# Optimization experiments

Measured on AMD Instinct MI355X. Metric: run time of the kernel, lower is better.

Reference implementation:

```python
import jax, jax.numpy as jnp
import numpy as np

DECAY = 0.99
EPS = 1e-10
COMMIT = 0.25
K = 1024
D = 64


def setup_inputs() -> dict:
    key = jax.random.key(0)
    k1, k2, k3, k4 = jax.random.split(key, 4)
    return {
        "z_e": jax.random.normal(k1, (64, 64, 32, 32), dtype=jnp.float32),
        "embedding_w": jax.random.normal(k2, (K, D), dtype=jnp.float32),
        "ema_cluster_size": jax.random.uniform(k3, (K,), dtype=jnp.float32),
        "ema_w": jax.random.normal(k4, (K, D), dtype=jnp.float32),
    }


def reference(z_e, embedding_w, ema_cluster_size, ema_w):
    # [B, C, H, W] -> [B, H, W, C] -> [N, D]
    z_nhwc = jnp.transpose(z_e, (0, 2, 3, 1))
    z_flat = z_nhwc.reshape(-1, z_nhwc.shape[-1])

    # Squared-euclidean distances via ||z||^2 + ||e||^2 - 2 z e^T  -> [N, K]
    z_sq = jnp.sum(z_flat * z_flat, axis=1, keepdims=True)
    e_sq = jnp.sum(embedding_w * embedding_w, axis=1)
    distances = z_sq + e_sq - 2.0 * (z_flat @ embedding_w.T)

    indices = jnp.argmin(distances, axis=1)                      # [N]
    encodings = jax.nn.one_hot(indices, K, dtype=z_flat.dtype)   # [N, K]

    quantized = embedding_w[indices].reshape(z_nhwc.shape)       # [B, H, W, C]

    # --- EMA codebook update (training path; no-grad in original) ---
    counts = jnp.sum(encodings, axis=0)                          # [K]
    new_cluster_size = DECAY * ema_cluster_size + (1.0 - DECAY) * counts
    dw = encodings.T @ z_flat                                    # [K, D]
    new_ema_w = DECAY * ema_w + (1.0 - DECAY) * dw
    n = jnp.sum(new_cluster_size)
    cluster_size = (new_cluster_size + EPS) / (n + K * EPS) * n
    new_embedding_w = new_ema_w / cluster_size[:, None]

    # Commitment loss (quantized detached)
    diff = jax.lax.stop_gradient(quantized) - z_nhwc
    loss = COMMIT * jnp.mean(diff * diff)

    # Straight-through estimator
    quantized_st = z_nhwc + jax.lax.stop_gradient(quantized - z_nhwc)

    avg_probs = jnp.mean(encodings, axis=0)
    perplexity = jnp.exp(-jnp.sum(avg_probs * jnp.log(avg_probs + 1e-10)))

    quantized_out = jnp.transpose(quantized_st, (0, 3, 1, 2))    # [B, C, H, W]
    return (quantized_out, loss, perplexity, encodings,
            new_embedding_w, new_cluster_size, new_ema_w)
```

## Files before the change

### kernel.cpp

```cpp
#include <hip/hip_runtime.h>
#include <math.h>

#define NTOT 65536
#define KCB  1024
#define DIM  64

typedef float fvec2 __attribute__((ext_vector_type(2)));
typedef float fvec4 __attribute__((ext_vector_type(4)));
typedef short sh8  __attribute__((ext_vector_type(8)));

static const size_t OFF_Q    = 0;
static const size_t OFF_LOSS = 4194304;
static const size_t OFF_PERP = 4194305;
static const size_t OFF_ENC  = 4194306;
static const size_t OFF_EMB  = 71303170;
static const size_t OFF_NCS  = 71368706;
static const size_t OFF_NEMA = 71369730;

static const size_t WSO_IDX   = 0;
static const size_t WSO_ESQ   = 262144;
static const size_t WSO_LOSSP = 266240;
static const size_t WSO_CNT   = 270336;
static const size_t WSO_SCAL  = 274432;
static const size_t WSO_EBH   = 278528;
static const size_t WSO_EBL   = 409600;
static const size_t WSO_PDW   = 540672;
static const size_t WSO_PCNT  = 4734976;
static const size_t WSO_ZC    = 4800512;
static const size_t WS_NEED_ZC = 4800512 + (size_t)NTOT * DIM * 4;

__device__ __forceinline__ unsigned short f2bf(float f) {
    unsigned u = __builtin_bit_cast(unsigned, f);
    return (unsigned short)((u + 0x7FFFu + ((u >> 16) & 1u)) >> 16);
}
__device__ __forceinline__ float bf2f(unsigned short h) {
    unsigned u = ((unsigned)h) << 16;
    return __builtin_bit_cast(float, u);
}

__global__ void k_eprep(const float* __restrict__ emb,
                        unsigned short* __restrict__ ebh,
                        unsigned short* __restrict__ ebl,
                        float* __restrict__ esq) {
    int gid = blockIdx.x * 256 + threadIdx.x;
    int c = gid >> 3, ko8 = gid & 7;
    const fvec4* p = (const fvec4*)(emb + ((size_t)c << 6) + (ko8 << 3));
    fvec4 v0 = p[0], v1 = p[1];
    float f[8] = {v0.x, v0.y, v0.z, v0.w, v1.x, v1.y, v1.z, v1.w};
    sh8 h, l;
    float sq0 = 0.f, sq1 = 0.f;
#pragma unroll
    for (int j = 0; j < 8; ++j) {
        unsigned short hb = f2bf(f[j]);
        h[j] = (short)hb;
        l[j] = (short)f2bf(f[j] - bf2f(hb));
        if (j < 4) sq0 = fmaf(f[j], f[j], sq0); else sq1 = fmaf(f[j], f[j], sq1);
    }
    float sq = sq0 + sq1;
    sq += __shfl_xor(sq, 1, 64);
    sq += __shfl_xor(sq, 2, 64);
    sq += __shfl_xor(sq, 4, 64);
    if (ko8 == 0) esq[c] = sq;

    int ct = c >> 4, cl = c & 15, kc = ko8 >> 2, ko = ko8 & 3;
    size_t base = ((((size_t)ct << 1) + kc) << 9) + (((size_t)(ko << 4) + cl) << 3);
    *(sh8*)(ebh + base) = h;
    *(sh8*)(ebl + base) = l;
}

__global__ __launch_bounds__(256, 4)
void k_assign(const float* __restrict__ ze, const float* __restrict__ emb,
              const float* __restrict__ esq,
              const unsigned short* __restrict__ ebh,
              const unsigned short* __restrict__ ebl,
              int* __restrict__ idx_out, float* __restrict__ lossp,
              float* __restrict__ zc, int use_zc) {
    __shared__ float zt[4096];
    __shared__ float etq[4096];
    __shared__ int   sfidx[64];

    const int tid  = threadIdx.x;
    const int blk  = blockIdx.x;
    const int b    = blk >> 4;
    const int hw0  = (blk & 15) << 6;
    const int n0   = blk << 6;
    const int lane = tid & 63;
    const int wave = tid >> 6;
    const int cg   = lane & 15;
    const int ko   = lane >> 4;

#pragma unroll
    for (int j = 0; j < 4; ++j) {
        int idx = tid + (j << 8);
        int d = idx >> 4, r0 = (idx & 15) << 2;
        const fvec4 v = *(const fvec4*)(ze + (((size_t)(b << 6) + d) << 10) + hw0 + r0);
        zt[(r0 + 0) * 64 + d] = v.x;
        zt[(r0 + 1) * 64 + d] = v.y;
        zt[(r0 + 2) * 64 + d] = v.z;
        zt[(r0 + 3) * 64 + d] = v.w;
    }
    __syncthreads();

    const int arow = (wave << 4) + cg;
    sh8 Ah0, Ah1, Al0, Al1;
#pragma unroll
    for (int j = 0; j < 8; ++j) {
        float f0 = zt[arow * 64 + (ko << 3) + j];
        float f1 = zt[arow * 64 + 32 + (ko << 3) + j];
        unsigned short h0 = f2bf(f0), h1 = f2bf(f1);
        Ah0[j] = (short)h0;  Al0[j] = (short)f2bf(f0 - bf2f(h0));
        Ah1[j] = (short)h1;  Al1[j] = (short)f2bf(f1 - bf2f(h1));
    }

    float tb[4]  = {3.4e38f, 3.4e38f, 3.4e38f, 3.4e38f};
    float ts2[4] = {3.4e38f, 3.4e38f, 3.4e38f, 3.4e38f};
    int ti1[4] = {0, 0, 0, 0};
    int ti2[4] = {0, 0, 0, 0};

    const size_t lb = (size_t)lane << 3;
#define LOADB(d0, d1, d2, d3, ctv)                                  \
    { size_t o_ = ((size_t)(ctv) << 10) + lb;                       \
      d0 = *(const sh8*)(ebh + o_);                                 \
      d1 = *(const sh8*)(ebh + o_ + 512);                           \
      d2 = *(const sh8*)(ebl + o_);                                 \
      d3 = *(const sh8*)(ebl + o_ + 512); }

#define FOLD(ctv, acc)                                              \
    { const int code_ = ((ctv) << 4) + cg;                          \
      const float es_ = esq[code_];                                 \
      _Pragma("unroll")                                             \
      for (int rg = 0; rg < 4; ++rg) {                              \
          float s_ = fmaf((acc)[rg], -2.0f, es_);                   \
          bool c1 = s_ < tb[rg];                                    \
          bool c2 = s_ < ts2[rg];                                   \
          ti2[rg] = c1 ? ti1[rg] : (c2 ? code_ : ti2[rg]);          \
          ts2[rg] = c1 ? tb[rg] : (c2 ? s_ : ts2[rg]);              \
          ti1[rg] = c1 ? code_ : ti1[rg];                           \
          tb[rg]  = c1 ? s_ : tb[rg];                               \
      } }

#define TILE(i) ((((i) + (blk << 1)) & 63))

    sh8 b0h0, b0h1, b0l0, b0l1, b1h0, b1h1, b1l0, b1l1;
    LOADB(b0h0, b0h1, b0l0, b0l1, TILE(0));
    LOADB(b1h0, b1h1, b1l0, b1l1, TILE(1));

    for (int i = 0; i < 64; i += 2) {
        fvec4 aa = {0.f, 0.f, 0.f, 0.f}, ab = {0.f, 0.f, 0.f, 0.f};
        aa = __builtin_amdgcn_mfma_f32_16x16x32_bf16(Ah0, b0h0, aa, 0, 0, 0);
        ab = __builtin_amdgcn_mfma_f32_16x16x32_bf16(Ah1, b0h1, ab, 0, 0, 0);
        aa = __builtin_amdgcn_mfma_f32_16x16x32_bf16(Ah0, b0l0, aa, 0, 0, 0);
        ab = __builtin_amdgcn_mfma_f32_16x16x32_bf16(Ah1, b0l1, ab, 0, 0, 0);
        aa = __builtin_amdgcn_mfma_f32_16x16x32_bf16(Al0, b0h0, aa, 0, 0, 0);
        ab = __builtin_amdgcn_mfma_f32_16x16x32_bf16(Al1, b0h1, ab, 0, 0, 0);
        const int ct0 = TILE(i);
        if (i + 2 < 64) LOADB(b0h0, b0h1, b0l0, b0l1, TILE(i + 2));
        fvec4 acc0 = aa + ab;
        FOLD(ct0, acc0);

        fvec4 ba = {0.f, 0.f, 0.f, 0.f}, bb = {0.f, 0.f, 0.f, 0.f};
        ba = __builtin_amdgcn_mfma_f32_16x16x32_bf16(Ah0, b1h0, ba, 0, 0, 0);
        bb = __builtin_amdgcn_mfma_f32_16x16x32_bf16(Ah1, b1h1, bb, 0, 0, 0);
        ba = __builtin_amdgcn_mfma_f32_16x16x32_bf16(Ah0, b1l0, ba, 0, 0, 0);
        bb = __builtin_amdgcn_mfma_f32_16x16x32_bf16(Ah1, b1l1, bb, 0, 0, 0);
        ba = __builtin_amdgcn_mfma_f32_16x16x32_bf16(Al0, b1h0, ba, 0, 0, 0);
        bb = __builtin_amdgcn_mfma_f32_16x16x32_bf16(Al1, b1h1, bb, 0, 0, 0);
        const int ct1 = TILE(i + 1);
        if (i + 3 < 64) LOADB(b1h0, b1h1, b1l0, b1l1, TILE(i + 3));
        fvec4 acc1 = ba + bb;
        FOLD(ct1, acc1);
    }
#undef TILE
#undef LOADB
#undef FOLD

    float* mb  = etq;
    float* ms2 = etq + 1024;
    int*   mi1 = (int*)(etq + 2048);
    int*   mi2 = (int*)(etq + 3072);
#pragma unroll
    for (int rg = 0; rg < 4; ++rg) {
        int row = (wave << 4) + (ko << 2) + rg;
        mb [(cg << 6) + row] = tb[rg];
        ms2[(cg << 6) + row] = ts2[rg];
        mi1[(cg << 6) + row] = ti1[rg];
        mi2[(cg << 6) + row] = ti2[rg];
    }
    __syncthreads();

    if (tid < 64) {
        const int r = tid;
        float fb = mb[r], fs2 = ms2[r];
        int fi1 = mi1[r], fi2 = mi2[r];
#pragma unroll
        for (int p = 1; p < 16; ++p) {
            float ob = mb[(p << 6) + r], os2 = ms2[(p << 6) + r];
            int oi1 = mi1[(p << 6) + r], oi2 = mi2[(p << 6) + r];
            if (ob < fb)       { fs2 = fb; fi2 = fi1; fb = ob; fi1 = oi1; }
            else if (ob < fs2) { fs2 = ob; fi2 = oi1; }
            if (os2 < fs2)     { fs2 = os2; fi2 = oi2; }
        }
        if (fs2 - fb < 2e-2f) {
            double d1 = 0.0, d2 = 0.0;
            const float* e1 = emb + (size_t)fi1 * 64;
            const float* e2 = emb + (size_t)fi2 * 64;
            for (int d = 0; d < 64; ++d) {
                double zd = (double)zt[r * 64 + d];
                double q1 = zd - (double)e1[d];
                double q2 = zd - (double)e2[d];
                d1 += q1 * q1;
                d2 += q2 * q2;
            }
            if ((d2 < d1) || (d2 == d1 && fi2 < fi1)) fi1 = fi2;
        }
        sfidx[r] = fi1;
        idx_out[n0 + r] = fi1;
    }
    __syncthreads();

    float lacc = 0.f;
    for (int i = tid; i < 1024; i += 256) {
        int r = i >> 4, d4 = (i & 15) << 2;
        const fvec4 zv = *(const fvec4*)&zt[(r << 6) + d4];
        const fvec4 ev = *(const fvec4*)(emb + ((size_t)sfidx[r] << 6) + d4);
        fvec4 df = ev - zv;
        lacc = fmaf(df.x, df.x, lacc);
        lacc = fmaf(df.y, df.y, lacc);
        lacc = fmaf(df.z, df.z, lacc);
        lacc = fmaf(df.w, df.w, lacc);
        if (use_zc)
            *(fvec4*)&zc[(((size_t)(n0 + r)) << 6) + d4] = zv;
    }
    __syncthreads();

    float* lred = etq;
    lred[tid] = lacc;
    __syncthreads();
    for (int s = 128; s > 0; s >>= 1) {
        if (tid < s) lred[tid] += lred[tid + s];
        __syncthreads();
    }
    if (tid == 0) lossp[blk] = lred[0];
}

__global__ __launch_bounds__(256)
void k_tail(const int* __restrict__ idx, const float* __restrict__ zcmp,
            const float* __restrict__ ze, const float* __restrict__ emb,
            float* __restrict__ out, float* __restrict__ pdw,
            int* __restrict__ pcnt, int use_zc) {
    __shared__ __align__(16) char smem[32864];
    const int t = threadIdx.x;

    if (blockIdx.x & 1) {
        const int blk = blockIdx.x >> 1;
        const int b   = blk >> 4;
        const int hw0 = (blk & 15) << 6;
        const int n0  = blk << 6;
        int*   sfidx = (int*)smem;
        float* qt    = (float*)(smem + 256);

        if (t < 64) sfidx[t] = idx[n0 + t];
        __syncthreads();

        for (int i = t; i < 4096; i += 256) {
            int r = i >> 6, d = i & 63;
            qt[d * 65 + r] = emb[(size_t)sfidx[r] * 64 + d];
        }

        float* ebase = out + OFF_ENC;
        if (t < 255) {
            const int cb = 2 + (t << 2);
            for (int r = 0; r < 64; ++r) {
                const int fi = sfidx[r];
                fvec4 v;
                v.x = (fi == cb)     ? 1.0f : 0.0f;
                v.y = (fi == cb + 1) ? 1.0f : 0.0f;
                v.z = (fi == cb + 2) ? 1.0f : 0.0f;
                v.w = (fi == cb + 3) ? 1.0f : 0.0f;
                __builtin_nontemporal_store(
                    v, (fvec4*)(ebase + ((size_t)(n0 + r) << 10) + cb));
            }
        } else {
            for (int r = 0; r < 64; ++r) {
                const int fi = sfidx[r];
                float* rowp = ebase + ((size_t)(n0 + r) << 10);
                fvec2 hd, tl;
                hd.x = (fi == 0)    ? 1.0f : 0.0f;
                hd.y = (fi == 1)    ? 1.0f : 0.0f;
                tl.x = (fi == 1022) ? 1.0f : 0.0f;
                tl.y = (fi == 1023) ? 1.0f : 0.0f;
                __builtin_nontemporal_store(hd, (fvec2*)rowp);
                __builtin_nontemporal_store(tl, (fvec2*)(rowp + 1022));
            }
        }
        __syncthreads();

        for (int i = t; i < 4096; i += 256) {
            int d = i >> 6, r = i & 63;
            __builtin_nontemporal_store(
                qt[d * 65 + r],
                &out[OFF_Q + ((size_t)((b << 6) + d) << 10) + hw0 + r]);
        }
        return;
    }

    const int sidx = blockIdx.x >> 1;
    const int kg   = sidx & 63;
    const int ng   = sidx >> 6;
    const int k0   = kg << 4;
    const int g    = t >> 6;
    const int d    = t & 63;
    const int lane = t & 63;

    int*   s_list = (int*)smem;
    float* part   = (float*)(smem + 16384);
    int*   s_wsum = (int*)(smem + 32768);
    int*   s_cnt  = (int*)(smem + 32784);

    for (int i = t; i < 4096; i += 256) part[i] = 0.f;
    if (t < 16) s_cnt[t] = 0;

    const int nb = (ng << 12) + (t << 4);
    const int4* ip = (const int4*)(idx + nb);
    const int4 v0 = ip[0], v1 = ip[1], v2 = ip[2], v3 = ip[3];

#define MM(x) ((unsigned)((x) - k0) < 16u)
    int c = 0;
    c += MM(v0.x) + MM(v0.y) + MM(v0.z) + MM(v0.w);
    c += MM(v1.x) + MM(v1.y) + MM(v1.z) + MM(v1.w);
    c += MM(v2.x) + MM(v2.y) + MM(v2.z) + MM(v2.w);
    c += MM(v3.x) + MM(v3.y) + MM(v3.z) + MM(v3.w);

    int inc = c;
#pragma unroll
    for (int off = 1; off < 64; off <<= 1) {
        int y = __shfl_up(inc, (unsigned)off, 64);
        if (lane >= off) inc += y;
    }
    if (lane == 63) s_wsum[g] = inc;
    __syncthreads();

    int wbase = 0;
#pragma unroll
    for (int w = 0; w < 4; ++w) wbase += (w < g) ? s_wsum[w] : 0;
    const int M = s_wsum[0] + s_wsum[1] + s_wsum[2] + s_wsum[3];
    int pos = wbase + inc - c;

#define EMIT(x, o) if (MM(x)) { s_list[pos++] = (((t << 4) + (o)) << 4) | ((x) - k0); \
                                atomicAdd(&s_cnt[(x) - k0], 1); }
    EMIT(v0.x, 0)  EMIT(v0.y, 1)  EMIT(v0.z, 2)  EMIT(v0.w, 3)
    EMIT(v1.x, 4)  EMIT(v1.y, 5)  EMIT(v1.z, 6)  EMIT(v1.w, 7)
    EMIT(v2.x, 8)  EMIT(v2.y, 9)  EMIT(v2.z, 10) EMIT(v2.w, 11)
    EMIT(v3.x, 12) EMIT(v3.y, 13) EMIT(v3.z, 14) EMIT(v3.w, 15)
#undef EMIT
#undef MM
    __syncthreads();

#define ZL(nloc) (use_zc ? zcmp[(((size_t)((ng << 12) + (nloc))) << 6) + d] \
                         : ze[((((size_t)(((ng << 12) + (nloc)) >> 10) << 6) + d) << 10) + (((ng << 12) + (nloc)) & 1023)])
    {
        float* pg = part + (g << 10);
        int j = g;
        for (; j + 4 < M; j += 8) {
            int e0 = s_list[j], e1 = s_list[j + 4];
            float f0 = ZL(e0 >> 4);
            float f1 = ZL(e1 >> 4);
            pg[((e0 & 15) << 6) + d] += f0;
            pg[((e1 & 15) << 6) + d] += f1;
        }
        for (; j < M; j += 4) {
            int e0 = s_list[j];
            pg[((e0 & 15) << 6) + d] += ZL(e0 >> 4);
        }
    }
#undef ZL
    __syncthreads();

    for (int i = t; i < 1024; i += 256) {
        float s = ((part[i] + part[1024 + i]) + part[2048 + i]) + part[3072 + i];
        int cc = i >> 6, dd = i & 63;
        pdw[(((size_t)(ng << 10) + k0 + cc) << 6) + dd] = s;
    }
    if (t < 16) pcnt[(ng << 10) + k0 + t] = s_cnt[t];
}

__global__ __launch_bounds__(256)
void k_red(const float* __restrict__ pdw, const int* __restrict__ pcnt,
           const float* __restrict__ emaw, const float* __restrict__ ecs,
           float* __restrict__ out, int* __restrict__ counts) {
    const int gid = blockIdx.x * 256 + threadIdx.x;
    const int k = gid >> 6, d = gid & 63;
    float s = 0.f;
#pragma unroll
    for (int ng = 0; ng < 16; ++ng)
        s += pdw[(((size_t)(ng << 10) + k) << 6) + d];
    out[OFF_NEMA + ((size_t)k << 6) + d] =
        fmaf(0.01f, s, 0.99f * emaw[((size_t)k << 6) + d]);
    if (d == 0) {
        int c = 0;
#pragma unroll
        for (int ng = 0; ng < 16; ++ng) c += pcnt[(ng << 10) + k];
        counts[k] = c;
        out[OFF_NCS + k] = fmaf(0.01f, (float)c, 0.99f * ecs[k]);
    }
}

__global__ void k_scalars(const float* __restrict__ lossp, const int* __restrict__ counts,
                          const float* __restrict__ ncs, float* __restrict__ out,
                          float* __restrict__ scal) {
    __shared__ float sr[256];
    const int t = threadIdx.x;

    float v = lossp[t] + lossp[t + 256] + lossp[t + 512] + lossp[t + 768];
    sr[t] = v;
    __syncthreads();
    for (int s = 128; s > 0; s >>= 1) { if (t < s) sr[t] += sr[t + s]; __syncthreads(); }
    if (t == 0) out[OFF_LOSS] = sr[0] * (0.25f / 4194304.0f);
    __syncthreads();

    v = ncs[t] + ncs[t + 256] + ncs[t + 512] + ncs[t + 768];
    sr[t] = v;
    __syncthreads();
    for (int s = 128; s > 0; s >>= 1) { if (t < s) sr[t] += sr[t + s]; __syncthreads(); }
    if (t == 0) scal[0] = sr[0];
    __syncthreads();

    float pv = 0.f;
    for (int i = t; i < 1024; i += 256) {
        float p = (float)counts[i] * (1.0f / 65536.0f);
        pv += p * logf(p + 1e-10f);
    }
    sr[t] = pv;
    __syncthreads();
    for (int s = 128; s > 0; s >>= 1) { if (t < s) sr[t] += sr[t + s]; __syncthreads(); }
    if (t == 0) out[OFF_PERP] = expf(-sr[0]);
}

__global__ void k_embnorm(const float* __restrict__ nema, const float* __restrict__ ncs,
                          const float* __restrict__ scal, float* __restrict__ embw) {
    int i = blockIdx.x * 256 + threadIdx.x;
    float n = scal[0];
    int k = i >> 6;
    float cs = (ncs[k] + 1e-10f) / (n + 1.024e-7f) * n;
    embw[i] = nema[i] / cs;
}

extern "C" void kernel_launch(void* const* d_in, const int* in_sizes, int n_in,
                              void* d_out, int out_size, void* d_ws, size_t ws_size,
                              hipStream_t stream) {
    const float* ze   = (const float*)d_in[0];
    const float* emb  = (const float*)d_in[1];
    const float* ecs  = (const float*)d_in[2];
    const float* emaw = (const float*)d_in[3];
    float* out = (float*)d_out;
    char*  ws  = (char*)d_ws;

    int*            idx    = (int*)(ws + WSO_IDX);
    float*          esq    = (float*)(ws + WSO_ESQ);
    float*          lossp  = (float*)(ws + WSO_LOSSP);
    int*            counts = (int*)(ws + WSO_CNT);
    float*          scal   = (float*)(ws + WSO_SCAL);
    unsigned short* ebh    = (unsigned short*)(ws + WSO_EBH);
    unsigned short* ebl    = (unsigned short*)(ws + WSO_EBL);
    float*          pdw    = (float*)(ws + WSO_PDW);
    int*            pcnt   = (int*)(ws + WSO_PCNT);
    float*          zc     = (float*)(ws + WSO_ZC);
    const int use_zc = (ws_size >= WS_NEED_ZC) ? 1 : 0;

    k_eprep  <<<32,   256, 0, stream>>>(emb, ebh, ebl, esq);
    k_assign <<<1024, 256, 0, stream>>>(ze, emb, esq, ebh, ebl, idx, lossp, zc, use_zc);
    k_tail   <<<2048, 256, 0, stream>>>(idx, zc, ze, emb, out, pdw, pcnt, use_zc);
    k_red    <<<256,  256, 0, stream>>>(pdw, pcnt, emaw, ecs, out, counts);
    k_scalars<<<1,    256, 0, stream>>>(lossp, counts, out + OFF_NCS, out, scal);
    k_embnorm<<<256,  256, 0, stream>>>(out + OFF_NEMA, out + OFF_NCS, scal, out + OFF_EMB);
}
```

Baseline: 155.1 us.

## Split assignment kernel into single-wave blocks of 16 rows with shuffle reductions

The codebook-assignment kernel moves from 256-thread blocks covering 64 rows to 64-thread single-wave blocks covering 16 rows, launched 4096 times. Cross-lane top-2 merging and the loss reduction now use wave shuffles instead of shared-memory tree reductions, which removes most barriers and shrinks LDS use so more blocks fit per CU. The explicit double-buffered codebook prefetch is dropped in favour of simple per-iteration loads. In exchange, each codebook tile is reloaded by four times as many blocks, the z loads become scalar strided reads, and the loss partial buffer grows to 4096 entries.

Measured after the change: 170.6 us. +10.0%, slower.

```diff
diff --git a/kernel.cpp b/kernel.cpp
--- a/kernel.cpp
+++ b/kernel.cpp
@@ -20,14 +20,14 @@
 static const size_t WSO_IDX   = 0;
 static const size_t WSO_ESQ   = 262144;
 static const size_t WSO_LOSSP = 266240;
-static const size_t WSO_CNT   = 270336;
-static const size_t WSO_SCAL  = 274432;
-static const size_t WSO_EBH   = 278528;
-static const size_t WSO_EBL   = 409600;
-static const size_t WSO_PDW   = 540672;
-static const size_t WSO_PCNT  = 4734976;
-static const size_t WSO_ZC    = 4800512;
-static const size_t WS_NEED_ZC = 4800512 + (size_t)NTOT * DIM * 4;
+static const size_t WSO_CNT   = 282624;
+static const size_t WSO_SCAL  = 286720;
+static const size_t WSO_EBH   = 290816;
+static const size_t WSO_EBL   = 421888;
+static const size_t WSO_PDW   = 552960;
+static const size_t WSO_PCNT  = 4747264;
+static const size_t WSO_ZC    = 4812800;
+static const size_t WS_NEED_ZC = 4812800 + (size_t)NTOT * DIM * 4;
 
 __device__ __forceinline__ unsigned short f2bf(float f) {
     unsigned u = __builtin_bit_cast(unsigned, f);
@@ -68,45 +68,40 @@
     *(sh8*)(ebl + base) = l;
 }
 
-__global__ __launch_bounds__(256, 4)
+__global__ __launch_bounds__(64, 8)
 void k_assign(const float* __restrict__ ze, const float* __restrict__ emb,
               const float* __restrict__ esq,
               const unsigned short* __restrict__ ebh,
               const unsigned short* __restrict__ ebl,
               int* __restrict__ idx_out, float* __restrict__ lossp,
               float* __restrict__ zc, int use_zc) {
-    __shared__ float zt[4096];
-    __shared__ float etq[4096];
-    __shared__ int   sfidx[64];
-
-    const int tid  = threadIdx.x;
+    __shared__ float zt[16 * 65];
+    __shared__ float sm_b[16], sm_s2[16];
+    __shared__ int   sm_i1[16], sm_i2[16], sfidx[16];
+
+    const int lane = threadIdx.x;
     const int blk  = blockIdx.x;
-    const int b    = blk >> 4;
-    const int hw0  = (blk & 15) << 6;
-    const int n0   = blk << 6;
-    const int lane = tid & 63;
-    const int wave = tid >> 6;
+    const int b    = blk >> 6;
+    const int hw0  = (blk & 63) << 4;
+    const int n0   = blk << 4;
     const int cg   = lane & 15;
     const int ko   = lane >> 4;
 
-#pragma unroll
-    for (int j = 0; j < 4; ++j) {
-        int idx = tid + (j << 8);
-        int d = idx >> 4, r0 = (idx & 15) << 2;
-        const fvec4 v = *(const fvec4*)(ze + (((size_t)(b << 6) + d) << 10) + hw0 + r0);
-        zt[(r0 + 0) * 64 + d] = v.x;
-        zt[(r0 + 1) * 64 + d] = v.y;
-        zt[(r0 + 2) * 64 + d] = v.z;
-        zt[(r0 + 3) * 64 + d] = v.w;
-    }
-    __syncthreads();
-
-    const int arow = (wave << 4) + cg;
+    {
+        const int r = lane & 15;
+        const int dq = lane >> 4;
+        for (int it = 0; it < 16; ++it) {
+            const int d = (it << 2) + dq;
+            zt[r * 65 + d] = ze[(((size_t)(b << 6) + d) << 10) + hw0 + r];
+        }
+    }
+    __syncthreads();
+
     sh8 Ah0, Ah1, Al0, Al1;
 #pragma unroll
     for (int j = 0; j < 8; ++j) {
-        float f0 = zt[arow * 64 + (ko << 3) + j];
-        float f1 = zt[arow * 64 + 32 + (ko << 3) + j];
+        float f0 = zt[cg * 65 + (ko << 3) + j];
+        float f1 = zt[cg * 65 + 32 + (ko << 3) + j];
         unsigned short h0 = f2bf(f0), h1 = f2bf(f1);
         Ah0[j] = (short)h0;  Al0[j] = (short)f2bf(f0 - bf2f(h0));
         Ah1[j] = (short)h1;  Al1[j] = (short)f2bf(f1 - bf2f(h1));
@@ -117,95 +112,75 @@
     int ti1[4] = {0, 0, 0, 0};
     int ti2[4] = {0, 0, 0, 0};
 
-    const size_t lb = (size_t)lane << 3;
-#define LOADB(d0, d1, d2, d3, ctv)                                  \
-    { size_t o_ = ((size_t)(ctv) << 10) + lb;                       \
-      d0 = *(const sh8*)(ebh + o_);                                 \
-      d1 = *(const sh8*)(ebh + o_ + 512);                           \
-      d2 = *(const sh8*)(ebl + o_);                                 \
-      d3 = *(const sh8*)(ebl + o_ + 512); }
-
-#define FOLD(ctv, acc)                                              \
-    { const int code_ = ((ctv) << 4) + cg;                          \
-      const float es_ = esq[code_];                                 \
-      _Pragma("unroll")                                             \
-      for (int rg = 0; rg < 4; ++rg) {                              \
-          float s_ = fmaf((acc)[rg], -2.0f, es_);                   \
-          bool c1 = s_ < tb[rg];                                    \
-          bool c2 = s_ < ts2[rg];                                   \
-          ti2[rg] = c1 ? ti1[rg] : (c2 ? code_ : ti2[rg]);          \
-          ts2[rg] = c1 ? tb[rg] : (c2 ? s_ : ts2[rg]);              \
-          ti1[rg] = c1 ? code_ : ti1[rg];                           \
-          tb[rg]  = c1 ? s_ : tb[rg];                               \
-      } }
-
-#define TILE(i) ((((i) + (blk << 1)) & 63))
-
-    sh8 b0h0, b0h1, b0l0, b0l1, b1h0, b1h1, b1l0, b1l1;
-    LOADB(b0h0, b0h1, b0l0, b0l1, TILE(0));
-    LOADB(b1h0, b1h1, b1l0, b1l1, TILE(1));
-
-    for (int i = 0; i < 64; i += 2) {
+    const int lb = lane << 3;
+
+    for (int i = 0; i < 64; ++i) {
+        const int ct = (i + blk) & 63;
+        const unsigned short* ph = ebh + ((size_t)ct << 10);
+        const unsigned short* pl = ebl + ((size_t)ct << 10);
+        sh8 bh0 = *(const sh8*)(ph + lb);
+        sh8 bh1 = *(const sh8*)(ph + 512 + lb);
+        sh8 bl0 = *(const sh8*)(pl + lb);
+        sh8 bl1 = *(const sh8*)(pl + 512 + lb);
+        const float es = esq[(ct << 4) + cg];
+
         fvec4 aa = {0.f, 0.f, 0.f, 0.f}, ab = {0.f, 0.f, 0.f, 0.f};
-        aa = __builtin_amdgcn_mfma_f32_16x16x32_bf16(Ah0, b0h0, aa, 0, 0, 0);
-        ab = __builtin_amdgcn_mfma_f32_16x16x32_bf16(Ah1, b0h1, ab, 0, 0, 0);
-        aa = __builtin_amdgcn_mfma_f32_16x16x32_bf16(Ah0, b0l0, aa, 0, 0, 0);
-        ab = __builtin_amdgcn_mfma_f32_16x16x32_bf16(Ah1, b0l1, ab, 0, 0, 0);
-        aa = __builtin_amdgcn_mfma_f32_16x16x32_bf16(Al0, b0h0, aa, 0, 0, 0);
-        ab = __builtin_amdgcn_mfma_f32_16x16x32_bf16(Al1, b0h1, ab, 0, 0, 0);
-        const int ct0 = TILE(i);
-        if (i + 2 < 64) LOADB(b0h0, b0h1, b0l0, b0l1, TILE(i + 2));
-        fvec4 acc0 = aa + ab;
-        FOLD(ct0, acc0);
-
-        fvec4 ba = {0.f, 0.f, 0.f, 0.f}, bb = {0.f, 0.f, 0.f, 0.f};
-        ba = __builtin_amdgcn_mfma_f32_16x16x32_bf16(Ah0, b1h0, ba, 0, 0, 0);
-        bb = __builtin_amdgcn_mfma_f32_16x16x32_bf16(Ah1, b1h1, bb, 0, 0, 0);
-        ba = __builtin_amdgcn_mfma_f32_16x16x32_bf16(Ah0, b1l0, ba, 0, 0, 0);
-        bb = __builtin_amdgcn_mfma_f32_16x16x32_bf16(Ah1, b1l1, bb, 0, 0, 0);
-        ba = __builtin_amdgcn_mfma_f32_16x16x32_bf16(Al0, b1h0, ba, 0, 0, 0);
-        bb = __builtin_amdgcn_mfma_f32_16x16x32_bf16(Al1, b1h1, bb, 0, 0, 0);
-        const int ct1 = TILE(i + 1);
-        if (i + 3 < 64) LOADB(b1h0, b1h1, b1l0, b1l1, TILE(i + 3));
-        fvec4 acc1 = ba + bb;
-        FOLD(ct1, acc1);
-    }
-#undef TILE
-#undef LOADB
-#undef FOLD
-
-    float* mb  = etq;
-    float* ms2 = etq + 1024;
-    int*   mi1 = (int*)(etq + 2048);
-    int*   mi2 = (int*)(etq + 3072);
-#pragma unroll
-    for (int rg = 0; rg < 4; ++rg) {
-        int row = (wave << 4) + (ko << 2) + rg;
-        mb [(cg << 6) + row] = tb[rg];
-        ms2[(cg << 6) + row] = ts2[rg];
-        mi1[(cg << 6) + row] = ti1[rg];
-        mi2[(cg << 6) + row] = ti2[rg];
-    }
-    __syncthreads();
-
-    if (tid < 64) {
-        const int r = tid;
-        float fb = mb[r], fs2 = ms2[r];
-        int fi1 = mi1[r], fi2 = mi2[r];
-#pragma unroll
-        for (int p = 1; p < 16; ++p) {
-            float ob = mb[(p << 6) + r], os2 = ms2[(p << 6) + r];
-            int oi1 = mi1[(p << 6) + r], oi2 = mi2[(p << 6) + r];
-            if (ob < fb)       { fs2 = fb; fi2 = fi1; fb = ob; fi1 = oi1; }
-            else if (ob < fs2) { fs2 = ob; fi2 = oi1; }
-            if (os2 < fs2)     { fs2 = os2; fi2 = oi2; }
-        }
-        if (fs2 - fb < 2e-2f) {
+        aa = __builtin_amdgcn_mfma_f32_16x16x32_bf16(Ah0, bh0, aa, 0, 0, 0);
+        ab = __builtin_amdgcn_mfma_f32_16x16x32_bf16(Ah1, bh1, ab, 0, 0, 0);
+        aa = __builtin_amdgcn_mfma_f32_16x16x32_bf16(Ah0, bl0, aa, 0, 0, 0);
+        ab = __builtin_amdgcn_mfma_f32_16x16x32_bf16(Ah1, bl1, ab, 0, 0, 0);
+        aa = __builtin_amdgcn_mfma_f32_16x16x32_bf16(Al0, bh0, aa, 0, 0, 0);
+        ab = __builtin_amdgcn_mfma_f32_16x16x32_bf16(Al1, bh1, ab, 0, 0, 0);
+        fvec4 acc = aa + ab;
+
+        const int code = (ct << 4) + cg;
+#pragma unroll
+        for (int s = 0; s < 4; ++s) {
+            float sc = fmaf(acc[s], -2.0f, es);
+            bool c1 = sc < tb[s];
+            bool c2 = sc < ts2[s];
+            ti2[s] = c1 ? ti1[s] : (c2 ? code : ti2[s]);
+            ts2[s] = c1 ? tb[s] : (c2 ? sc : ts2[s]);
+            ti1[s] = c1 ? code : ti1[s];
+            tb[s]  = c1 ? sc : tb[s];
+        }
+    }
+
+#pragma unroll
+    for (int s = 0; s < 4; ++s) {
+#pragma unroll
+        for (int st = 1; st < 16; st <<= 1) {
+            float ob  = __shfl_xor(tb[s],  st, 64);
+            float os2 = __shfl_xor(ts2[s], st, 64);
+            int   oi1 = __shfl_xor(ti1[s], st, 64);
+            int   oi2 = __shfl_xor(ti2[s], st, 64);
+            if (ob < tb[s]) { ts2[s] = tb[s]; ti2[s] = ti1[s]; tb[s] = ob; ti1[s] = oi1; }
+            else if (ob < ts2[s]) { ts2[s] = ob; ti2[s] = oi1; }
+            if (os2 < ts2[s]) { ts2[s] = os2; ti2[s] = oi2; }
+        }
+    }
+    if (cg == 0) {
+#pragma unroll
+        for (int s = 0; s < 4; ++s) {
+            const int row = (ko << 2) + s;
+            sm_b[row]  = tb[s];
+            sm_s2[row] = ts2[s];
+            sm_i1[row] = ti1[s];
+            sm_i2[row] = ti2[s];
+        }
+    }
+    __syncthreads();
+
+    if (lane < 16) {
+        const int r = lane;
+        int fi1 = sm_i1[r];
+        if (sm_s2[r] - sm_b[r] < 2e-2f) {
+            int fi2 = sm_i2[r];
             double d1 = 0.0, d2 = 0.0;
             const float* e1 = emb + (size_t)fi1 * 64;
             const float* e2 = emb + (size_t)fi2 * 64;
             for (int d = 0; d < 64; ++d) {
-                double zd = (double)zt[r * 64 + d];
+                double zd = (double)zt[r * 65 + d];
                 double q1 = zd - (double)e1[d];
                 double q2 = zd - (double)e2[d];
                 d1 += q1 * q1;
@@ -219,28 +194,30 @@
     __syncthreads();
 
     float lacc = 0.f;
-    for (int i = tid; i < 1024; i += 256) {
-        int r = i >> 4, d4 = (i & 15) << 2;
-        const fvec4 zv = *(const fvec4*)&zt[(r << 6) + d4];
-        const fvec4 ev = *(const fvec4*)(emb + ((size_t)sfidx[r] << 6) + d4);
-        fvec4 df = ev - zv;
-        lacc = fmaf(df.x, df.x, lacc);
-        lacc = fmaf(df.y, df.y, lacc);
-        lacc = fmaf(df.z, df.z, lacc);
-        lacc = fmaf(df.w, df.w, lacc);
-        if (use_zc)
-            *(fvec4*)&zc[(((size_t)(n0 + r)) << 6) + d4] = zv;
-    }
-    __syncthreads();
-
-    float* lred = etq;
-    lred[tid] = lacc;
-    __syncthreads();
-    for (int s = 128; s > 0; s >>= 1) {
-        if (tid < s) lred[tid] += lred[tid + s];
-        __syncthreads();
-    }
-    if (tid == 0) lossp[blk] = lred[0];
+    {
+        const int r  = lane >> 2;
+        const int d0 = (lane & 3) << 4;
+        const float* er = emb + ((size_t)sfidx[r] << 6) + d0;
+        float zrow[16];
+#pragma unroll
+        for (int j = 0; j < 16; ++j) {
+            float zv = zt[r * 65 + d0 + j];
+            zrow[j] = zv;
+            float df = er[j] - zv;
+            lacc = fmaf(df, df, lacc);
+        }
+        if (use_zc) {
+            float* zp = zc + (((size_t)(n0 + r)) << 6) + d0;
+#pragma unroll
+            for (int j = 0; j < 4; ++j) {
+                fvec4 v = {zrow[4*j], zrow[4*j+1], zrow[4*j+2], zrow[4*j+3]};
+                *(fvec4*)(zp + (j << 2)) = v;
+            }
+        }
+    }
+#pragma unroll
+    for (int st = 1; st < 64; st <<= 1) lacc += __shfl_xor(lacc, st, 64);
+    if (lane == 0) lossp[blk] = lacc;
 }
 
 __global__ __launch_bounds__(256)
@@ -411,7 +388,8 @@
     __shared__ float sr[256];
     const int t = threadIdx.x;
 
-    float v = lossp[t] + lossp[t + 256] + lossp[t + 512] + lossp[t + 768];
+    float v = 0.f;
+    for (int i = t; i < 4096; i += 256) v += lossp[i];
     sr[t] = v;
     __syncthreads();
     for (int s = 128; s > 0; s >>= 1) { if (t < s) sr[t] += sr[t + s]; __syncthreads(); }
@@ -468,7 +446,7 @@
     const int use_zc = (ws_size >= WS_NEED_ZC) ? 1 : 0;
 
     k_eprep  <<<32,   256, 0, stream>>>(emb, ebh, ebl, esq);
-    k_assign <<<1024, 256, 0, stream>>>(ze, emb, esq, ebh, ebl, idx, lossp, zc, use_zc);
+    k_assign <<<4096, 64,  0, stream>>>(ze, emb, esq, ebh, ebl, idx, lossp, zc, use_zc);
     k_tail   <<<2048, 256, 0, stream>>>(idx, zc, ze, emb, out, pdw, pcnt, use_zc);
     k_red    <<<256,  256, 0, stream>>>(pdw, pcnt, emaw, ecs, out, counts);
     k_scalars<<<1,    256, 0, stream>>>(lossp, counts, out + OFF_NCS, out, scal);
```
